# Optimization experiments

Hardware: AMD Instinct MI355X
Metric: run time of the kernel (lower is better)

Reference implementation:

```python
import jax, jax.numpy as jnp
import numpy as np


def setup_inputs() -> dict:
    key = jax.random.key(0)
    k1, k2, k3 = jax.random.split(key, 3)
    N, C, H, W = 4, 2048, 32, 48
    feature = jax.random.normal(k1, (N, C, H, W), dtype=jnp.float32)
    # Conv2d(C, C, (1, 9)) weight/bias; small scale so the 48-step recurrence stays finite
    conv_w = jax.random.normal(k2, (C, C, 1, 9), dtype=jnp.float32) * 0.01
    conv_b = jax.random.normal(k3, (C,), dtype=jnp.float32) * 0.01
    prelu_a = jnp.asarray(0.25, dtype=jnp.float32)  # nn.PReLU() default single param
    return {"feature": feature, "conv_w": conv_w, "conv_b": conv_b, "prelu_a": prelu_a}


def reference(feature, conv_w, conv_b, prelu_a):
    # feature: [N, C, H, W]
    # Each recurrence step applies Conv2d(kernel=(1,9), pad=(0,4)) to a width-1
    # slice [N,C,H,1]: after padding to width 9, only the center tap (kw=4)
    # overlaps the data, so conv(x) == W[:,:,0,4] @ x + b exactly.
    Wc = conv_w[:, :, 0, 4]  # [C_out, C_in]

    def step(prev, x_i):
        # prev, x_i: [N, C, H]
        y = jnp.einsum('oc,nch->noh', Wc, prev) + conv_b[None, :, None]
        y = jnp.where(y >= 0, y, prelu_a * y)  # PReLU
        cur = y + x_i
        return cur, cur

    x = jnp.moveaxis(feature, 3, 0)  # [W, N, C, H]

    # Left-to-right pass: F[0] = x[0]; F[i] = prelu(conv(F[i-1])) + x[i]
    _, fwd_rest = jax.lax.scan(step, x[0], x[1:])
    fl = jnp.concatenate([x[0:1], fwd_rest], axis=0)  # [W, N, C, H]

    # Right-to-left pass: F[W-1] unchanged; F[i] = prelu(conv(F[i+1])) + F[i]
    _, bwd_rest = jax.lax.scan(step, fl[-1], fl[:-1], reverse=True)
    out = jnp.concatenate([bwd_rest, fl[-1:]], axis=0)  # [W, N, C, H]

    return jnp.moveaxis(out, 0, 3)  # [N, C, H, W]
```

## Files before the change

kernel.cpp:

```cpp
#include <hip/hip_runtime.h>

#define CH   2048
#define COLS 128
#define WDIM 48
#define SL   (COLS*CH)
#define NWG  256
#define TPB  512

using f32x4  = __attribute__((ext_vector_type(4))) float;
using bf16x8 = __attribute__((ext_vector_type(8))) short;

__device__ __forceinline__ short f2bf(float f) {
    union { float f; unsigned u; } v; v.f = f;
    unsigned u = v.u;
    u += 0x7fffu + ((u >> 16) & 1u);
    return (short)(u >> 16);
}

__global__ __launch_bounds__(256) void prep_w(const float* __restrict__ cw,
                                              short* __restrict__ wcb) {
    int idx = blockIdx.x * 256 + threadIdx.x;
    wcb[idx] = f2bf(cw[(size_t)idx * 9 + 4]);
}

__global__ __launch_bounds__(256) void prep_x(const float* __restrict__ feat,
                                              float* __restrict__ xt) {
    int b = blockIdx.x;
    int col = b >> 5;
    int ct  = b & 31;
    int n = col >> 5, h = col & 31;
    int c0 = ct * 64;
    __shared__ float tile[64][49];
    int t = threadIdx.x;
    const float* base = feat + (((size_t)n * CH + c0) * 32 + h) * WDIM;
    #pragma unroll
    for (int it = 0; it < 3; ++it) {
        int id = it * 256 + t;
        int row = id / 12, w4 = id % 12;
        float4 v = *reinterpret_cast<const float4*>(base + (size_t)row * 1536 + w4 * 4);
        tile[row][w4*4+0] = v.x; tile[row][w4*4+1] = v.y;
        tile[row][w4*4+2] = v.z; tile[row][w4*4+3] = v.w;
    }
    __syncthreads();
    int c = t & 63, wq = t >> 6;
    #pragma unroll
    for (int it = 0; it < 12; ++it) {
        int w = it * 4 + wq;
        xt[((size_t)w * COLS + col) * CH + c0 + c] = tile[c][w];
    }
}

__global__ __launch_bounds__(256) void init0_k(const float* __restrict__ x0,
                                               float* __restrict__ fl0,
                                               short* __restrict__ fb0) {
    int i = blockIdx.x * 256 + threadIdx.x;
    float v = x0[i];
    fl0[i] = v;
    fb0[i] = f2bf(v);
}

__global__ __launch_bounds__(TPB, 1) void persist_k(
        const short* __restrict__ wcb, const float* __restrict__ xt,
        short* __restrict__ flbf, short* __restrict__ bwdb,
        float* __restrict__ fl32, float* __restrict__ outt,
        const float* __restrict__ bias, const float* __restrict__ pa,
        unsigned* flags, int byp)
{
    __shared__ float red[8 * 16 * 65];
    __shared__ short sst[16 * 68];

    int wg = blockIdx.x;
    int grp = wg & 7;
    int mg  = wg >> 3;
    int n0 = grp * 16;
    int m0 = mg * 64;
    int t = threadIdx.x;
    int wv = t >> 6, l = t & 63;
    int lc = l & 15;
    int lg = l >> 4;

    bf16x8 aR[4][8];
    {
        const short* ab = wcb + (size_t)(m0 + lc) * CH + wv * 256 + 8 * lg;
        #pragma unroll
        for (int rb = 0; rb < 4; ++rb)
            #pragma unroll
            for (int ks = 0; ks < 8; ++ks)
                aR[rb][ks] = *reinterpret_cast<const bf16x8*>(ab + (size_t)rb * 16 * CH + ks * 32);
    }

    int rb0 = wv >> 2, reg = wv & 3;
    int row0 = rb0 * 16 + lg * 4 + reg;
    size_t off0 = (size_t)(n0 + lc) * CH + m0 + row0;
    size_t off1 = off0 + 32;
    float b0 = bias[m0 + row0], b1 = bias[m0 + row0 + 32];
    float aP = *pa;
    size_t soff = (((size_t)(n0 + (t >> 5)) * CH + m0) >> 1) + (t & 31);
    size_t boffs = (size_t)(n0 + lc) * CH + wv * 256 + 8 * lg;

    unsigned* gflags = flags + grp * 64;

    auto waitflags = [&](unsigned sc) {
        int guard = 0;
        for (;;) {
            unsigned v = __hip_atomic_load(gflags + (l & 31),
                                           __ATOMIC_RELAXED, __HIP_MEMORY_SCOPE_AGENT);
            if (__all((int)(v >= sc))) break;
            __builtin_amdgcn_s_sleep(1);
            if (++guard > (1 << 20)) break;
        }
    };
    auto post = [&](unsigned sc) {
        __syncthreads();
        if (t == 0)
            __hip_atomic_store(gflags + mg, sc,
                               __ATOMIC_RELAXED, __HIP_MEMORY_SCOPE_AGENT);
    };

    float lastv0 = 0.f, lastv1 = 0.f;

    auto step = [&](const short* prevb, const float* res, float* outf,
                    short* outb, bool dostate, bool bypass, unsigned scwait) {
        float r0 = res[off0], r1 = res[off1];
        if (scwait) waitflags(scwait);
        bf16x8 bq[8];
        const short* bp = prevb + boffs;
        if (!bypass) {
            #pragma unroll
            for (int ks = 0; ks < 8; ++ks)
                bq[ks] = *reinterpret_cast<const bf16x8*>(bp + ks * 32);
        } else {
            #pragma unroll
            for (int ks = 0; ks < 8; ++ks) {
                union { int i4[4]; bf16x8 v; } u;
                const int* ip = reinterpret_cast<const int*>(bp + ks * 32);
                #pragma unroll
                for (int j = 0; j < 4; ++j)
                    u.i4[j] = __hip_atomic_load(const_cast<int*>(ip) + j,
                                                __ATOMIC_RELAXED, __HIP_MEMORY_SCOPE_AGENT);
                bq[ks] = u.v;
            }
        }
        f32x4 acc[4] = {};
        #pragma unroll
        for (int ks = 0; ks < 8; ++ks)
            #pragma unroll
            for (int rb = 0; rb < 4; ++rb)
                acc[rb] = __builtin_amdgcn_mfma_f32_16x16x32_bf16(
                              aR[rb][ks], bq[ks], acc[rb], 0, 0, 0);
        #pragma unroll
        for (int rb = 0; rb < 4; ++rb)
            #pragma unroll
            for (int rg = 0; rg < 4; ++rg)
                red[wv * 1040 + (rb * 4 + rg) * 65 + l] = acc[rb][rg];
        __syncthreads();
        float s0 = 0.f, s1 = 0.f;
        #pragma unroll
        for (int w2 = 0; w2 < 8; ++w2) {
            s0 += red[w2 * 1040 + wv * 65 + l];
            s1 += red[w2 * 1040 + (wv + 8) * 65 + l];
        }
        float v0 = s0 + b0; v0 = (v0 >= 0.f) ? v0 : aP * v0; v0 += r0;
        float v1 = s1 + b1; v1 = (v1 >= 0.f) ? v1 : aP * v1; v1 += r1;
        outf[off0] = v0; outf[off1] = v1;
        lastv0 = v0; lastv1 = v1;
        if (dostate) {
            sst[lc * 68 + row0]      = f2bf(v0);
            sst[lc * 68 + row0 + 32] = f2bf(v1);
            __syncthreads();
            int sv = reinterpret_cast<const int*>(sst)[(t >> 5) * 34 + (t & 31)];
            __hip_atomic_store(reinterpret_cast<int*>(outb) + soff, sv,
                               __ATOMIC_RELAXED, __HIP_MEMORY_SCOPE_AGENT);
        }
    };

    for (int w = 1; w <= 47; ++w) {
        step(flbf + (size_t)(w - 1) * SL, xt + (size_t)w * SL,
             fl32 + (size_t)w * SL, flbf + (size_t)w * SL,
             true, false, (unsigned)(w - 1));
        post((unsigned)w);
    }
    outt[(size_t)47 * SL + off0] = lastv0;
    outt[(size_t)47 * SL + off1] = lastv1;
    const short* prev = flbf + (size_t)47 * SL;
    unsigned sc = 47;
    for (int i = 46; i >= 0; --i) {
        short* nxt = bwdb + (size_t)(byp ? (i & 1) : i) * SL;
        bool st = (i > 0);
        step(prev, fl32 + (size_t)i * SL, outt + (size_t)i * SL,
             nxt, st, byp && (i < 46), sc);
        if (st) { ++sc; post(sc); }
        prev = nxt;
    }
}

__global__ __launch_bounds__(256) void fin_t(const float* __restrict__ ot,
                                             float* __restrict__ dout) {
    int b = blockIdx.x;
    int col = b >> 5, ct = b & 31;
    int n = col >> 5, h = col & 31;
    int c0 = ct * 64;
    __shared__ float tile[48][65];
    int t = threadIdx.x;
    int c = t & 63, wq = t >> 6;
    #pragma unroll
    for (int it = 0; it < 12; ++it) {
        int w = it * 4 + wq;
        tile[w][c] = ot[((size_t)w * COLS + col) * CH + c0 + c];
    }
    __syncthreads();
    float* base = dout + (((size_t)n * CH + c0) * 32 + h) * WDIM;
    #pragma unroll
    for (int it = 0; it < 3; ++it) {
        int id = it * 256 + t;
        int row = id / 12, w4 = id % 12;
        float4 v;
        v.x = tile[w4*4+0][row]; v.y = tile[w4*4+1][row];
        v.z = tile[w4*4+2][row]; v.w = tile[w4*4+3][row];
        *reinterpret_cast<float4*>(base + (size_t)row * 1536 + w4 * 4) = v;
    }
}

extern "C" void kernel_launch(void* const* d_in, const int* in_sizes, int n_in,
                              void* d_out, int out_size, void* d_ws, size_t ws_size,
                              hipStream_t stream) {
    const float* feat = (const float*)d_in[0];
    const float* cw   = (const float*)d_in[1];
    const float* bias = (const float*)d_in[2];
    const float* pa   = (const float*)d_in[3];

    float* fl32 = (float*)d_out;

    char* ws = (char*)d_ws;
    short* wcb  = (short*)(ws);
    float* xt   = (float*)(ws + 8388608);
    short* flbf = (short*)(ws + 58720256);
    unsigned* flags = (unsigned*)(ws + 83886080);
    short* bwdb = (short*)(ws + 83888128);
    float* outt = xt;

    const size_t needed_full = 83888128ull + 47ull * SL * 2;
    int byp = (ws_size < needed_full) ? 1 : 0;

    hipMemsetAsync(flags, 0, 2048, stream);
    prep_w<<<16384, 256, 0, stream>>>(cw, wcb);
    prep_x<<<4096, 256, 0, stream>>>(feat, xt);
    init0_k<<<1024, 256, 0, stream>>>(xt, fl32, flbf);

    persist_k<<<NWG, TPB, 0, stream>>>(wcb, xt, flbf, bwdb, fl32, outt,
                                       bias, pa, flags, byp);

    fin_t<<<4096, 256, 0, stream>>>(outt, (float*)d_out);
}
```

Before: 431.4 us.

## Split persistent workgroups over two column groups to overlap flag waits

Each persistent workgroup now owns 32 output channels for two 16-column groups instead of 64 channels for one group. The two groups are processed alternately, so while one group's dependency flags resolve the other can compute. The flag post is deferred and folded into the next phase's barrier. Flags grow to 64 producers per group, and each workgroup now holds half the weight registers. The cost is more flag polling and more steps per workgroup, each doing less MFMA work.

```diff
diff --git a/kernel.cpp b/kernel.cpp
--- a/kernel.cpp
+++ b/kernel.cpp
@@ -64,67 +64,60 @@
         short* __restrict__ flbf, short* __restrict__ bwdb,
         float* __restrict__ fl32, float* __restrict__ outt,
         const float* __restrict__ bias, const float* __restrict__ pa,
-        unsigned* flags, int byp)
+        unsigned* __restrict__ flags, int byp)
 {
-    __shared__ float red[8 * 16 * 65];
-    __shared__ short sst[16 * 68];
+    __shared__ float red[8 * 8 * 65];
+    __shared__ short sst[16 * 36];
 
     int wg = blockIdx.x;
-    int grp = wg & 7;
-    int mg  = wg >> 3;
-    int n0 = grp * 16;
-    int m0 = mg * 64;
+    int pr = wg & 3;
+    int mg = wg >> 2;
+    int m0 = mg * 32;
+    int gA = pr * 2, gB = pr * 2 + 1;
     int t = threadIdx.x;
     int wv = t >> 6, l = t & 63;
-    int lc = l & 15;
-    int lg = l >> 4;
-
-    bf16x8 aR[4][8];
+    int lc = l & 15, lg = l >> 4;
+
+    bf16x8 aR[2][8];
     {
         const short* ab = wcb + (size_t)(m0 + lc) * CH + wv * 256 + 8 * lg;
         #pragma unroll
-        for (int rb = 0; rb < 4; ++rb)
+        for (int rb = 0; rb < 2; ++rb)
             #pragma unroll
             for (int ks = 0; ks < 8; ++ks)
                 aR[rb][ks] = *reinterpret_cast<const bf16x8*>(ab + (size_t)rb * 16 * CH + ks * 32);
     }
 
-    int rb0 = wv >> 2, reg = wv & 3;
-    int row0 = rb0 * 16 + lg * 4 + reg;
-    size_t off0 = (size_t)(n0 + lc) * CH + m0 + row0;
-    size_t off1 = off0 + 32;
-    float b0 = bias[m0 + row0], b1 = bias[m0 + row0 + 32];
+    int row0 = (wv >> 2) * 16 + lg * 4 + (wv & 3);
+    int o0 = m0 + row0;
+    float b0v = bias[o0];
     float aP = *pa;
-    size_t soff = (((size_t)(n0 + (t >> 5)) * CH + m0) >> 1) + (t & 31);
-    size_t boffs = (size_t)(n0 + lc) * CH + wv * 256 + 8 * lg;
-
-    unsigned* gflags = flags + grp * 64;
-
-    auto waitflags = [&](unsigned sc) {
-        int guard = 0;
-        for (;;) {
-            unsigned v = __hip_atomic_load(gflags + (l & 31),
-                                           __ATOMIC_RELAXED, __HIP_MEMORY_SCOPE_AGENT);
-            if (__all((int)(v >= sc))) break;
-            __builtin_amdgcn_s_sleep(1);
-            if (++guard > (1 << 20)) break;
+
+    int n0A = gA * 16, n0B = gB * 16;
+    size_t off0A = (size_t)(n0A + lc) * CH + o0;
+    size_t off0B = (size_t)(n0B + lc) * CH + o0;
+    size_t boffsA = (size_t)(n0A + lc) * CH + wv * 256 + 8 * lg;
+    size_t boffsB = (size_t)(n0B + lc) * CH + wv * 256 + 8 * lg;
+    size_t soffA = (((size_t)(n0A + (t >> 4)) * CH + m0) >> 1) + (t & 15);
+    size_t soffB = (((size_t)(n0B + (t >> 4)) * CH + m0) >> 1) + (t & 15);
+
+    int pendG = -1; unsigned pendV = 0;
+
+    auto corePhase = [&](int g, size_t boffs, const short* src,
+                         unsigned pollval, float r0, bool bypass) -> float {
+        if (pollval) {
+            const unsigned* f = flags + g * 64 + wv * 8 + (l & 7);
+            int guard = 0;
+            for (;;) {
+                unsigned v = __hip_atomic_load(f, __ATOMIC_RELAXED, __HIP_MEMORY_SCOPE_AGENT);
+                if (__all((int)(v >= pollval))) break;
+                __builtin_amdgcn_s_sleep(1);
+                if (++guard > (1 << 20)) break;
+            }
+            __builtin_amdgcn_sched_barrier(0);
         }
-    };
-    auto post = [&](unsigned sc) {
-        __syncthreads();
-        if (t == 0)
-            __hip_atomic_store(gflags + mg, sc,
-                               __ATOMIC_RELAXED, __HIP_MEMORY_SCOPE_AGENT);
-    };
-
-    float lastv0 = 0.f, lastv1 = 0.f;
-
-    auto step = [&](const short* prevb, const float* res, float* outf,
-                    short* outb, bool dostate, bool bypass, unsigned scwait) {
-        float r0 = res[off0], r1 = res[off1];
-        if (scwait) waitflags(scwait);
         bf16x8 bq[8];
-        const short* bp = prevb + boffs;
+        const short* bp = src + boffs;
         if (!bypass) {
             #pragma unroll
             for (int ks = 0; ks < 8; ++ks)
@@ -141,56 +134,78 @@
                 bq[ks] = u.v;
             }
         }
-        f32x4 acc[4] = {};
+        f32x4 acc[2] = {};
         #pragma unroll
         for (int ks = 0; ks < 8; ++ks)
             #pragma unroll
-            for (int rb = 0; rb < 4; ++rb)
+            for (int rb = 0; rb < 2; ++rb)
                 acc[rb] = __builtin_amdgcn_mfma_f32_16x16x32_bf16(
                               aR[rb][ks], bq[ks], acc[rb], 0, 0, 0);
-        #pragma unroll
-        for (int rb = 0; rb < 4; ++rb)
+        __syncthreads();
+        if (pendG >= 0 && t == 0)
+            __hip_atomic_store(flags + pendG * 64 + mg, pendV,
+                               __ATOMIC_RELAXED, __HIP_MEMORY_SCOPE_AGENT);
+        #pragma unroll
+        for (int rb = 0; rb < 2; ++rb)
             #pragma unroll
             for (int rg = 0; rg < 4; ++rg)
-                red[wv * 1040 + (rb * 4 + rg) * 65 + l] = acc[rb][rg];
+                red[wv * 520 + (rb * 4 + rg) * 65 + l] = acc[rb][rg];
         __syncthreads();
-        float s0 = 0.f, s1 = 0.f;
-        #pragma unroll
-        for (int w2 = 0; w2 < 8; ++w2) {
-            s0 += red[w2 * 1040 + wv * 65 + l];
-            s1 += red[w2 * 1040 + (wv + 8) * 65 + l];
-        }
-        float v0 = s0 + b0; v0 = (v0 >= 0.f) ? v0 : aP * v0; v0 += r0;
-        float v1 = s1 + b1; v1 = (v1 >= 0.f) ? v1 : aP * v1; v1 += r1;
-        outf[off0] = v0; outf[off1] = v1;
-        lastv0 = v0; lastv1 = v1;
-        if (dostate) {
-            sst[lc * 68 + row0]      = f2bf(v0);
-            sst[lc * 68 + row0 + 32] = f2bf(v1);
-            __syncthreads();
-            int sv = reinterpret_cast<const int*>(sst)[(t >> 5) * 34 + (t & 31)];
-            __hip_atomic_store(reinterpret_cast<int*>(outb) + soff, sv,
+        float s0 = 0.f;
+        #pragma unroll
+        for (int w2 = 0; w2 < 8; ++w2) s0 += red[w2 * 520 + wv * 65 + l];
+        float v = s0 + b0v; v = (v >= 0.f) ? v : aP * v; v += r0;
+        return v;
+    };
+
+    auto publish = [&](short* dst, size_t soff_, float v) {
+        sst[lc * 36 + row0] = f2bf(v);
+        __syncthreads();
+        if (t < 256) {
+            int sv = reinterpret_cast<const int*>(sst)[(t >> 4) * 18 + (t & 15)];
+            __hip_atomic_store(reinterpret_cast<int*>(dst) + soff_, sv,
                                __ATOMIC_RELAXED, __HIP_MEMORY_SCOPE_AGENT);
         }
     };
 
+    float vA = 0.f, vB = 0.f;
+
     for (int w = 1; w <= 47; ++w) {
-        step(flbf + (size_t)(w - 1) * SL, xt + (size_t)w * SL,
-             fl32 + (size_t)w * SL, flbf + (size_t)w * SL,
-             true, false, (unsigned)(w - 1));
-        post((unsigned)w);
-    }
-    outt[(size_t)47 * SL + off0] = lastv0;
-    outt[(size_t)47 * SL + off1] = lastv1;
-    const short* prev = flbf + (size_t)47 * SL;
-    unsigned sc = 47;
+        float rA = xt[(size_t)w * SL + off0A];
+        vA = corePhase(gA, boffsA, flbf + (size_t)(w - 1) * SL,
+                       (unsigned)(w - 1), rA, false);
+        fl32[(size_t)w * SL + off0A] = vA;
+        publish(flbf + (size_t)w * SL, soffA, vA);
+        pendG = gA; pendV = (unsigned)w;
+
+        float rB = xt[(size_t)w * SL + off0B];
+        vB = corePhase(gB, boffsB, flbf + (size_t)(w - 1) * SL,
+                       (unsigned)(w - 1), rB, false);
+        fl32[(size_t)w * SL + off0B] = vB;
+        publish(flbf + (size_t)w * SL, soffB, vB);
+        pendG = gB; pendV = (unsigned)w;
+    }
+    outt[(size_t)47 * SL + off0A] = vA;
+    outt[(size_t)47 * SL + off0B] = vB;
+
     for (int i = 46; i >= 0; --i) {
+        const short* src = (i == 46) ? flbf + (size_t)47 * SL
+                                     : bwdb + (size_t)(byp ? ((i + 1) & 1) : (i + 1)) * SL;
+        unsigned pv = (i == 46) ? 47u : (unsigned)(93 - i);
+        bool byl = byp && (i < 45);
         short* nxt = bwdb + (size_t)(byp ? (i & 1) : i) * SL;
-        bool st = (i > 0);
-        step(prev, fl32 + (size_t)i * SL, outt + (size_t)i * SL,
-             nxt, st, byp && (i < 46), sc);
-        if (st) { ++sc; post(sc); }
-        prev = nxt;
+
+        float rA = fl32[(size_t)i * SL + off0A];
+        vA = corePhase(gA, boffsA, src, pv, rA, byl);
+        outt[(size_t)i * SL + off0A] = vA;
+        if (i > 0) { publish(nxt, soffA, vA);
+                     pendG = gA; pendV = (unsigned)(94 - i); }
+
+        float rB = fl32[(size_t)i * SL + off0B];
+        vB = corePhase(gB, boffsB, src, pv, rB, byl);
+        outt[(size_t)i * SL + off0B] = vB;
+        if (i > 0) { publish(nxt, soffB, vB);
+                     pendG = gB; pendV = (unsigned)(94 - i); }
     }
 }
 
@@ -236,13 +251,13 @@
     float* xt   = (float*)(ws + 8388608);
     short* flbf = (short*)(ws + 58720256);
     unsigned* flags = (unsigned*)(ws + 83886080);
-    short* bwdb = (short*)(ws + 83888128);
+    short* bwdb = (short*)(ws + 83890176);
     float* outt = xt;
 
-    const size_t needed_full = 83888128ull + 47ull * SL * 2;
+    const size_t needed_full = 83890176ull + 47ull * SL * 2;
     int byp = (ws_size < needed_full) ? 1 : 0;
 
-    hipMemsetAsync(flags, 0, 2048, stream);
+    hipMemsetAsync(flags, 0, 4096, stream);
     prep_w<<<16384, 256, 0, stream>>>(cw, wcb);
     prep_x<<<4096, 256, 0, stream>>>(feat, xt);
     init0_k<<<1024, 256, 0, stream>>>(xt, fl32, flbf);
```

Result: slower. 636.1 us (+47.5%).

## Use per-wave flags and double-buffered reduction to cut per-step barriers

Applied to the files above, without the earlier changes.

Replaces the per-workgroup flag post, which needed a __syncthreads before publishing, with per-wave flags. Each wave packs its two bf16 outputs and publishes them straight to global memory, then sets its own flag after a vmcnt wait. The reduction buffer is double-buffered so the next step can begin without a second barrier, and the staging shared array is removed. Consumers poll 32 flags per wave instead of waiting on a workgroup post. This shortens the serial critical path of the 94-step recurrence, at the cost of more flag traffic and more polling.

```diff
diff --git a/kernel.cpp b/kernel.cpp
--- a/kernel.cpp
+++ b/kernel.cpp
@@ -64,20 +64,17 @@
         short* __restrict__ flbf, short* __restrict__ bwdb,
         float* __restrict__ fl32, float* __restrict__ outt,
         const float* __restrict__ bias, const float* __restrict__ pa,
-        unsigned* flags, int byp)
+        unsigned* __restrict__ flags, int byp)
 {
-    __shared__ float red[8 * 16 * 65];
-    __shared__ short sst[16 * 68];
+    __shared__ float red[2][8 * 16 * 65];
 
     int wg = blockIdx.x;
     int grp = wg & 7;
     int mg  = wg >> 3;
-    int n0 = grp * 16;
-    int m0 = mg * 64;
+    int n0 = grp * 16, m0 = mg * 64;
     int t = threadIdx.x;
     int wv = t >> 6, l = t & 63;
-    int lc = l & 15;
-    int lg = l >> 4;
+    int lc = l & 15, lg = l >> 4;
 
     bf16x8 aR[4][8];
     {
@@ -89,42 +86,43 @@
                 aR[rb][ks] = *reinterpret_cast<const bf16x8*>(ab + (size_t)rb * 16 * CH + ks * 32);
     }
 
-    int rb0 = wv >> 2, reg = wv & 3;
-    int row0 = rb0 * 16 + lg * 4 + reg;
-    size_t off0 = (size_t)(n0 + lc) * CH + m0 + row0;
-    size_t off1 = off0 + 32;
-    float b0 = bias[m0 + row0], b1 = bias[m0 + row0 + 32];
+    int c = l >> 2, j = l & 3;
+    int r0 = wv * 8 + j * 2, r1 = r0 + 1;
+    size_t eoff = (size_t)(n0 + c) * CH + m0 + r0;
+    float2 bias2 = *reinterpret_cast<const float2*>(bias + m0 + r0);
     float aP = *pa;
-    size_t soff = (((size_t)(n0 + (t >> 5)) * CH + m0) >> 1) + (t & 31);
+    size_t poff = (((size_t)(n0 + c) * CH + m0) >> 1) + wv * 4 + j;
     size_t boffs = (size_t)(n0 + lc) * CH + wv * 256 + 8 * lg;
 
-    unsigned* gflags = flags + grp * 64;
-
-    auto waitflags = [&](unsigned sc) {
+    int slot0 = ((r0 >> 4) << 2) + (r0 & 3), ls0 = (((r0 >> 2) & 3) << 4) + c;
+    int slot1 = ((r1 >> 4) << 2) + (r1 & 3), ls1 = (((r1 >> 2) & 3) << 4) + c;
+
+    unsigned* gf = flags + grp * 256;
+    int pidx = (l < 32) ? ((wv * 4 + (l >> 3)) * 8 + (l & 7)) : 0;
+    unsigned* myflag = gf + mg * 8 + wv;
+
+    auto poll = [&](unsigned tgt) {
         int guard = 0;
         for (;;) {
-            unsigned v = __hip_atomic_load(gflags + (l & 31),
-                                           __ATOMIC_RELAXED, __HIP_MEMORY_SCOPE_AGENT);
-            if (__all((int)(v >= sc))) break;
-            __builtin_amdgcn_s_sleep(1);
-            if (++guard > (1 << 20)) break;
-        }
+            unsigned v = __hip_atomic_load(gf + pidx, __ATOMIC_RELAXED,
+                                           __HIP_MEMORY_SCOPE_AGENT);
+            int ok = (l >= 32) | (v >= tgt);
+            if (__all(ok)) break;
+            if (++guard > (1 << 17)) break;
+        }
+        __builtin_amdgcn_sched_barrier(0);
     };
-    auto post = [&](unsigned sc) {
-        __syncthreads();
-        if (t == 0)
-            __hip_atomic_store(gflags + mg, sc,
-                               __ATOMIC_RELAXED, __HIP_MEMORY_SCOPE_AGENT);
-    };
-
-    float lastv0 = 0.f, lastv1 = 0.f;
-
-    auto step = [&](const short* prevb, const float* res, float* outf,
-                    short* outb, bool dostate, bool bypass, unsigned scwait) {
-        float r0 = res[off0], r1 = res[off1];
-        if (scwait) waitflags(scwait);
+
+    float v0 = 0.f, v1 = 0.f;
+    int par = 0;
+
+    auto phase = [&](const short* src, unsigned pollval, const float* resp,
+                     float* flw, float* outw, short* pubw, unsigned postval,
+                     bool bypass) {
+        float2 res = *reinterpret_cast<const float2*>(resp + eoff);
+        if (pollval) poll(pollval);
         bf16x8 bq[8];
-        const short* bp = prevb + boffs;
+        const short* bp = src + boffs;
         if (!bypass) {
             #pragma unroll
             for (int ks = 0; ks < 8; ++ks)
@@ -135,9 +133,9 @@
                 union { int i4[4]; bf16x8 v; } u;
                 const int* ip = reinterpret_cast<const int*>(bp + ks * 32);
                 #pragma unroll
-                for (int j = 0; j < 4; ++j)
-                    u.i4[j] = __hip_atomic_load(const_cast<int*>(ip) + j,
-                                                __ATOMIC_RELAXED, __HIP_MEMORY_SCOPE_AGENT);
+                for (int q2 = 0; q2 < 4; ++q2)
+                    u.i4[q2] = __hip_atomic_load(const_cast<int*>(ip) + q2,
+                                 __ATOMIC_RELAXED, __HIP_MEMORY_SCOPE_AGENT);
                 bq[ks] = u.v;
             }
         }
@@ -148,49 +146,63 @@
             for (int rb = 0; rb < 4; ++rb)
                 acc[rb] = __builtin_amdgcn_mfma_f32_16x16x32_bf16(
                               aR[rb][ks], bq[ks], acc[rb], 0, 0, 0);
+        float* rw = &red[par][0];
         #pragma unroll
         for (int rb = 0; rb < 4; ++rb)
             #pragma unroll
             for (int rg = 0; rg < 4; ++rg)
-                red[wv * 1040 + (rb * 4 + rg) * 65 + l] = acc[rb][rg];
+                rw[wv * 1040 + (rb * 4 + rg) * 65 + l] = acc[rb][rg];
         __syncthreads();
         float s0 = 0.f, s1 = 0.f;
         #pragma unroll
         for (int w2 = 0; w2 < 8; ++w2) {
-            s0 += red[w2 * 1040 + wv * 65 + l];
-            s1 += red[w2 * 1040 + (wv + 8) * 65 + l];
-        }
-        float v0 = s0 + b0; v0 = (v0 >= 0.f) ? v0 : aP * v0; v0 += r0;
-        float v1 = s1 + b1; v1 = (v1 >= 0.f) ? v1 : aP * v1; v1 += r1;
-        outf[off0] = v0; outf[off1] = v1;
-        lastv0 = v0; lastv1 = v1;
-        if (dostate) {
-            sst[lc * 68 + row0]      = f2bf(v0);
-            sst[lc * 68 + row0 + 32] = f2bf(v1);
-            __syncthreads();
-            int sv = reinterpret_cast<const int*>(sst)[(t >> 5) * 34 + (t & 31)];
-            __hip_atomic_store(reinterpret_cast<int*>(outb) + soff, sv,
+            s0 += rw[w2 * 1040 + slot0 * 65 + ls0];
+            s1 += rw[w2 * 1040 + slot1 * 65 + ls1];
+        }
+        v0 = s0 + bias2.x; v0 = (v0 >= 0.f) ? v0 : aP * v0; v0 += res.x;
+        v1 = s1 + bias2.y; v1 = (v1 >= 0.f) ? v1 : aP * v1; v1 += res.y;
+        if (flw)  { float2 o{v0, v1}; *reinterpret_cast<float2*>(flw + eoff) = o; }
+        if (outw) { float2 o{v0, v1}; *reinterpret_cast<float2*>(outw + eoff) = o; }
+        if (pubw) {
+            unsigned pv = (unsigned)(unsigned short)f2bf(v0)
+                        | ((unsigned)(unsigned short)f2bf(v1) << 16);
+            __hip_atomic_store(reinterpret_cast<int*>(pubw) + poff, (int)pv,
                                __ATOMIC_RELAXED, __HIP_MEMORY_SCOPE_AGENT);
-        }
+            asm volatile("s_waitcnt vmcnt(0)" ::: "memory");
+            if (l == 0)
+                __hip_atomic_store(myflag, postval, __ATOMIC_RELAXED,
+                                   __HIP_MEMORY_SCOPE_AGENT);
+        }
+        par ^= 1;
     };
 
-    for (int w = 1; w <= 47; ++w) {
-        step(flbf + (size_t)(w - 1) * SL, xt + (size_t)w * SL,
-             fl32 + (size_t)w * SL, flbf + (size_t)w * SL,
-             true, false, (unsigned)(w - 1));
-        post((unsigned)w);
-    }
-    outt[(size_t)47 * SL + off0] = lastv0;
-    outt[(size_t)47 * SL + off1] = lastv1;
-    const short* prev = flbf + (size_t)47 * SL;
-    unsigned sc = 47;
+    for (int w = 1; w <= 47; ++w)
+        phase(flbf + (size_t)(w - 1) * SL, (unsigned)(w - 1),
+              xt + (size_t)w * SL, fl32 + (size_t)w * SL, nullptr,
+              flbf + (size_t)w * SL, (unsigned)w, false);
+
+    {
+        int guard = 0;
+        for (;;) {
+            unsigned v = __hip_atomic_load(gf + ((wv * 32 + l) & 255),
+                                           __ATOMIC_RELAXED, __HIP_MEMORY_SCOPE_AGENT);
+            int ok = (l >= 32) | (v >= 47u);
+            if (__all(ok)) break;
+            if (++guard > (1 << 17)) break;
+        }
+        __syncthreads();
+        float2 o{v0, v1};
+        *reinterpret_cast<float2*>(outt + (size_t)47 * SL + eoff) = o;
+    }
+
     for (int i = 46; i >= 0; --i) {
-        short* nxt = bwdb + (size_t)(byp ? (i & 1) : i) * SL;
-        bool st = (i > 0);
-        step(prev, fl32 + (size_t)i * SL, outt + (size_t)i * SL,
-             nxt, st, byp && (i < 46), sc);
-        if (st) { ++sc; post(sc); }
-        prev = nxt;
+        const short* src = (i == 46) ? flbf + (size_t)47 * SL
+                                     : bwdb + (size_t)(byp ? ((i + 1) & 1) : (i + 1)) * SL;
+        unsigned pvw = (i == 46) ? 47u : (unsigned)(93 - i);
+        bool byl = byp && (i < 45);
+        short* pub = (i > 0) ? bwdb + (size_t)(byp ? (i & 1) : i) * SL : nullptr;
+        phase(src, pvw, fl32 + (size_t)i * SL, nullptr,
+              outt + (size_t)i * SL, pub, (unsigned)(94 - i), byl);
     }
 }
 
@@ -236,13 +248,13 @@
     float* xt   = (float*)(ws + 8388608);
     short* flbf = (short*)(ws + 58720256);
     unsigned* flags = (unsigned*)(ws + 83886080);
-    short* bwdb = (short*)(ws + 83888128);
+    short* bwdb = (short*)(ws + 83894272);
     float* outt = xt;
 
-    const size_t needed_full = 83888128ull + 47ull * SL * 2;
+    const size_t needed_full = 83894272ull + 47ull * SL * 2;
     int byp = (ws_size < needed_full) ? 1 : 0;
 
-    hipMemsetAsync(flags, 0, 2048, stream);
+    hipMemsetAsync(flags, 0, 8192, stream);
     prep_w<<<16384, 256, 0, stream>>>(cw, wcb);
     prep_x<<<4096, 256, 0, stream>>>(feat, xt);
     init0_k<<<1024, 256, 0, stream>>>(xt, fl32, flbf);
```

New measurement: 1.083 ms. 151% more time.
